# Optimization experiments

Measured on AMD Instinct MI355X. Metric: run time of the kernel, lower is better.

The kernel has to match this reference:

```python
import jax, jax.numpy as jnp
import numpy as np

B, T, H = 256, 48, 512   # batch, timesteps, hidden (= size_seq feature dim)
S = H                    # size_seq == hidden feature dim (dim_seq_in = S+1)
K = 4                    # k_wk_ahead


def setup_inputs() -> dict:
    key = jax.random.key(0)
    ks = jax.random.split(key, 20)
    g = lambda k, shp: (jax.random.normal(k, shp, dtype=jnp.float32) * 0.05)
    inp = {
        "hiddens": jax.random.normal(ks[0], (B, T, S), dtype=jnp.float32),
        "allys": jax.random.normal(ks[1], (B, T), dtype=jnp.float32),
        "k_wk_ahead": K,
        # InputAttention params (Linear stored as [in, out])
        "Wh": g(ks[2], (H, S)), "bh": g(ks[3], (S,)),
        "Ws": g(ks[4], (S, S)), "bs": g(ks[5], (S,)),
        "Wo": g(ks[6], (S, 1)), "bo": g(ks[7], (1,)),
        # GRU params (torch layout: [3H, in]/[3H, H], gates ordered r,z,n)
        "W_ih": g(ks[8], (3 * H, S + 1)), "W_hh": g(ks[9], (3 * H, H)),
        "b_ih": g(ks[10], (3 * H,)), "b_hh": g(ks[11], (3 * H,)),
        # out_layer MLP: H->H/2->H/4->H/8->1 with LeakyReLU after each
        "W1": g(ks[12], (H, H // 2)), "b1": g(ks[13], (H // 2,)),
        "W2": g(ks[14], (H // 2, H // 4)), "b2": g(ks[15], (H // 4,)),
        "W3": g(ks[16], (H // 4, H // 8)), "b3": g(ks[17], (H // 8,)),
        "W4": g(ks[18], (H // 8, 1)), "b4": g(ks[19], (1,)),
    }
    return inp


def _gru_step(x, h, W_ih, W_hh, b_ih, b_hh):
    # torch GRU cell: gates ordered (reset, update, new)
    gi = x @ W_ih.T + b_ih          # [B, 3H]
    gh = h @ W_hh.T + b_hh          # [B, 3H]
    ir, iz, inn = jnp.split(gi, 3, axis=-1)
    hr, hz, hn = jnp.split(gh, 3, axis=-1)
    r = jax.nn.sigmoid(ir + hr)
    z = jax.nn.sigmoid(iz + hz)
    n = jnp.tanh(inn + r * hn)
    return (1.0 - z) * n + z * h


def reference(hiddens, allys, k_wk_ahead, Wh, bh, Ws, bs, Wo, bo,
              W_ih, W_hh, b_ih, b_hh, W1, b1, W2, b2, W3, b3, W4, b4):
    Bb, Tt, Ss = hiddens.shape
    # linearSignals(hiddens) is time-step-invariant: precompute once
    ls = hiddens @ Ws + bs                      # [B, T, S]

    def step(d_prev, ally_t):
        lh = d_prev @ Wh + bh                   # [B, S]
        e = jnp.tanh(lh[:, None, :] + ls) @ Wo + bo    # [B, T, 1]
        att = jax.nn.softmax(e, axis=1)[..., 0]        # [B, T]
        c = jnp.einsum('bt,bts->bs', att, hiddens)     # [B, S]
        x = jnp.concatenate([c, ally_t[:, None]], axis=1)   # [B, S+1]
        d = _gru_step(x, d_prev, W_ih, W_hh, b_ih, b_hh)
        return d, c

    d0 = jnp.zeros((Bb, W_hh.shape[1]), dtype=hiddens.dtype)
    d_last, cs = jax.lax.scan(step, d0, jnp.swapaxes(allys, 0, 1))
    c_last = cs[-1]                             # c_vectors[:, -1]

    def mlp(d):
        h = jax.nn.leaky_relu(d @ W1 + b1)
        h = jax.nn.leaky_relu(h @ W2 + b2)
        h = jax.nn.leaky_relu(h @ W3 + b3)
        return jax.nn.leaky_relu(h @ W4 + b4)   # dropout is identity in eval

    outs = []
    last_d = d_last
    for _ in range(k_wk_ahead):
        out = mlp(last_d)                       # [B, 1]
        outs.append(out)
        x = jnp.concatenate([c_last, out], axis=1)
        last_d = _gru_step(x, last_d, W_ih, W_hh, b_ih, b_hh)
    return jnp.stack(outs, axis=1)[..., 0]      # [B, K]
```

## Files before the change

### kernel.cpp

```cpp
#include <hip/hip_runtime.h>
#include <cstdio>

#ifndef __has_builtin
#define __has_builtin(x) 0
#endif

#define NB      256
#define NT      48
#define NS      512
#define KAHEAD  4
#define NTHREADS 1024
#define NBLOCKS  256
#define GSIZE    32
#define RSTRIDE  544
#define XSLOT    512
#define XROWB    1088

#define WS_D     0
#define WS_X     139264
#define WS_LH    278528
#define WS_BAR   409600
#define WS_WA    409856
#define WS_WC    934144
#define WS_WN    1196288
#define WS_WS    1327360
#define WS_FLOATS 1458432

#define L_XHI    0
#define L_XLO    34816
#define L_LSB    69632
#define L_GH     118784
#define L_GI     125312
#define L_LH     131840
#define L_WO     133888
#define L_E      135936
#define L_ATT    136192
#define L_CP     136448
#define L_H1P    138496
#define L_H1S    142592
#define L_H2P    143616
#define L_H2S    145664
#define L_H3P    146176
#define L_MISC   147200
#define L_PB     147216
#define LDS_BYTES 155408

typedef float    f4v  __attribute__((ext_vector_type(4)));
typedef float    f16v __attribute__((ext_vector_type(16)));
typedef _Float16 h4v  __attribute__((ext_vector_type(4)));
typedef _Float16 h8v  __attribute__((ext_vector_type(8)));

__device__ __forceinline__ f16v MFMA32(h8v a, h8v b, f16v c) {
    return __builtin_amdgcn_mfma_f32_32x32x16_f16(a, b, c, 0, 0, 0);
}
__device__ __forceinline__ f4v MFMA16(h8v a, h8v b, f4v c) {
    return __builtin_amdgcn_mfma_f32_16x16x32_f16(a, b, c, 0, 0, 0);
}

__device__ __forceinline__ float frcp_(float x) {
#if __has_builtin(__builtin_amdgcn_rcpf)
    return __builtin_amdgcn_rcpf(x);
#else
    return 1.0f / x;
#endif
}
__device__ __forceinline__ float ftanh_(float x) {
    float e = __expf(2.0f * x);
    return 1.0f - 2.0f * frcp_(e + 1.0f);
}
__device__ __forceinline__ float fsig_(float x) { return frcp_(1.0f + __expf(-x)); }
__device__ __forceinline__ float lrelu_(float x) { return fmaxf(x, 0.01f * x); }
__device__ __forceinline__ unsigned short rne16_(unsigned u) {
    return (unsigned short)((u + 0x7FFFu + ((u >> 16) & 1u)) >> 16);
}
__device__ __forceinline__ float bf2f_(unsigned short b) {
    return __uint_as_float(((unsigned)b) << 16);
}
__device__ __forceinline__ void split16_(float v, _Float16& hi, _Float16& lo) {
    _Float16 h = (_Float16)v;
    hi = h;
    lo = (_Float16)(v - (float)h);
}

__device__ __forceinline__ void cstore1(float* p, float v) {
    asm volatile("global_store_dword %0, %1, off sc0 nt" :: "v"(p), "v"(v) : "memory");
}
__device__ __forceinline__ f4v cload4(const float* p) {
    f4v v;
    asm volatile("global_load_dwordx4 %0, %1, off sc0" : "=v"(v) : "v"(p));
    return v;
}
__device__ __forceinline__ float cload1(const float* p) {
    float v;
    asm volatile("global_load_dword %0, %1, off sc0" : "=v"(v) : "v"(p));
    return v;
}
__device__ __forceinline__ void cwait() {
    asm volatile("s_waitcnt vmcnt(0)" ::: "memory");
    __builtin_amdgcn_sched_barrier(0);
}

__device__ __forceinline__ void gbar(unsigned* bar, unsigned* epoch) {
    asm volatile("s_waitcnt vmcnt(0)" ::: "memory");
    __syncthreads();
    if (threadIdx.x == 0) {
        *epoch += GSIZE;
        __hip_atomic_fetch_add(bar, 1u, __ATOMIC_RELAXED, __HIP_MEMORY_SCOPE_AGENT);
        unsigned target = *epoch;
        int guard = 0;
        while (__hip_atomic_load(bar, __ATOMIC_RELAXED, __HIP_MEMORY_SCOPE_AGENT) < target) {
#if __has_builtin(__builtin_amdgcn_s_sleep)
            __builtin_amdgcn_s_sleep(2);
#endif
            if (++guard > (1 << 16)) break;
        }
    }
    __syncthreads();
}

__device__ __forceinline__ void cvtStore_(char* hiB, char* loB, int idx, f4v v) {
    unsigned row = (unsigned)idx / 544u;
    unsigned col = (unsigned)idx - row * 544u;
    h4v h, l;
    #pragma unroll
    for (int i = 0; i < 4; ++i) { _Float16 hh, ll; split16_(v[i], hh, ll); h[i] = hh; l[i] = ll; }
    *(h4v*)(hiB + row * XROWB + col * 2) = h;
    *(h4v*)(loB + row * XROWB + col * 2) = l;
}
__device__ __forceinline__ void stagePanel(const float* __restrict__ gsrc,
                                           char* __restrict__ hiB,
                                           char* __restrict__ loB, int tid) {
    f4v v0 = cload4(gsrc + tid * 4);
    f4v v1 = cload4(gsrc + 4096 + tid * 4);
    f4v v2 = cload4(gsrc + 8192 + tid * 4);
    f4v v3 = cload4(gsrc + 12288 + tid * 4);
    f4v v4 = {0.f, 0.f, 0.f, 0.f};
    if (tid < 256) v4 = cload4(gsrc + 16384 + tid * 4);
    cwait();
    cvtStore_(hiB, loB, tid * 4, v0);
    cvtStore_(hiB, loB, 4096 + tid * 4, v1);
    cvtStore_(hiB, loB, 8192 + tid * 4, v2);
    cvtStore_(hiB, loB, 12288 + tid * 4, v3);
    if (tid < 256) cvtStore_(hiB, loB, 16384 + tid * 4, v4);
}

__device__ __forceinline__ void gemmA(const char* smem, const _Float16* WA_,
        int cix, int g, int tid, float* ghs, float* lhw, float* pbuf,
        const float* bh, const float* bhh, bool doLH) {
    const int w = tid >> 6, l = tid & 63;
    const int nt2 = w & 1, kc = w >> 1;
    f16v acc = {0,0,0,0,0,0,0,0,0,0,0,0,0,0,0,0};
    if (w < 4) {
        const int aoff = (l & 31) * XROWB + ((l >> 5) << 4);
        const _Float16* Bp = WA_ + ((long)((cix * 2 + nt2) * 32 + kc * 16)) * 512 + (l << 3);
        #pragma unroll 4
        for (int kt = 0; kt < 16; ++kt) {
            h8v ah = *(const h8v*)(smem + L_XHI + aoff + (kc * 16 + kt) * 32);
            h8v al = *(const h8v*)(smem + L_XLO + aoff + (kc * 16 + kt) * 32);
            h8v b  = *(const h8v*)(Bp + kt * 512);
            acc = MFMA32(ah, b, acc);
            acc = MFMA32(al, b, acc);
        }
        if (kc == 1) {
            #pragma unroll
            for (int r = 0; r < 16; ++r) pbuf[nt2 * 1024 + r * 64 + l] = acc[r];
        }
    }
    __syncthreads();
    if (w < 2) {
        #pragma unroll
        for (int r = 0; r < 16; ++r) acc[r] += pbuf[nt2 * 1024 + r * 64 + l];
        const int c = nt2 * 32 + (l & 31);
        const int rb = (l >> 5) << 2;
        if (c < 16) {
            if (doLH) {
                const int j = cix * 16 + c;
                const float b = bh[j];
                #pragma unroll
                for (int r = 0; r < 16; ++r) {
                    int row = (r & 3) + ((r >> 2) << 3) + rb;
                    cstore1(lhw + (long)(g * 32 + row) * NS + j, acc[r] + b);
                }
            }
        } else {
            const int gate = (c - 16) >> 4, jj = (c - 16) & 15;
            const float b = bhh[gate * 512 + cix * 16 + jj];
            #pragma unroll
            for (int r = 0; r < 16; ++r) {
                int row = (r & 3) + ((r >> 2) << 3) + rb;
                ghs[gate * 544 + row * 17 + jj] = acc[r] + b;
            }
        }
    }
}

__device__ __forceinline__ void gemmC(const char* smem, const _Float16* WC_,
        const _Float16* WN_, int cix, int tid, float* gis, float* pbuf,
        const float* bih) {
    const int w = tid >> 6, l = tid & 63;
    f16v acc = {0,0,0,0,0,0,0,0,0,0,0,0,0,0,0,0};
    f4v an0 = {0.f,0.f,0.f,0.f}, an1 = {0.f,0.f,0.f,0.f};
    if (w < 2) {
        const int aoff = (l & 31) * XROWB + ((l >> 5) << 4);
        const _Float16* Bp = WC_ + ((long)(cix * 32 + w * 16)) * 512 + (l << 3);
        #pragma unroll 4
        for (int kt = 0; kt < 16; ++kt) {
            h8v ah = *(const h8v*)(smem + L_XHI + aoff + (w * 16 + kt) * 32);
            h8v al = *(const h8v*)(smem + L_XLO + aoff + (w * 16 + kt) * 32);
            h8v b  = *(const h8v*)(Bp + kt * 512);
            acc = MFMA32(ah, b, acc);
            acc = MFMA32(al, b, acc);
        }
        if (w == 1) {
            #pragma unroll
            for (int r = 0; r < 16; ++r) pbuf[r * 64 + l] = acc[r];
        }
    } else if (w < 4) {
        const int kc = w - 2;
        const _Float16* Bp = WN_ + ((long)(cix * 16 + kc * 8)) * 512 + (l << 3);
        const int a0 = (l & 15) * XROWB + ((l >> 4) << 4);
        const int a1 = (16 + (l & 15)) * XROWB + ((l >> 4) << 4);
        #pragma unroll 4
        for (int kt = 0; kt < 8; ++kt) {
            const int kb = (kc * 8 + kt) * 64;
            h8v b   = *(const h8v*)(Bp + kt * 512);
            h8v ah0 = *(const h8v*)(smem + L_XHI + a0 + kb);
            h8v al0 = *(const h8v*)(smem + L_XLO + a0 + kb);
            h8v ah1 = *(const h8v*)(smem + L_XHI + a1 + kb);
            h8v al1 = *(const h8v*)(smem + L_XLO + a1 + kb);
            an0 = MFMA16(ah0, b, an0); an0 = MFMA16(al0, b, an0);
            an1 = MFMA16(ah1, b, an1); an1 = MFMA16(al1, b, an1);
        }
        if (kc == 1) {
            #pragma unroll
            for (int r = 0; r < 4; ++r) {
                pbuf[1024 + r * 64 + l] = an0[r];
                pbuf[1280 + r * 64 + l] = an1[r];
            }
        }
    }
    __syncthreads();
    if (w == 0) {
        #pragma unroll
        for (int r = 0; r < 16; ++r) acc[r] += pbuf[r * 64 + l];
        const int c = l & 31, gate = c >> 4, jj = c & 15;
        const int rb = (l >> 5) << 2;
        const float b = bih[gate * 512 + cix * 16 + jj];
        #pragma unroll
        for (int r = 0; r < 16; ++r) {
            int row = (r & 3) + ((r >> 2) << 3) + rb;
            gis[gate * 544 + row * 17 + jj] = acc[r] + b;
        }
    } else if (w == 2) {
        const int jj = l & 15;
        const float b = bih[1024 + cix * 16 + jj];
        #pragma unroll
        for (int r = 0; r < 4; ++r) {
            int row = ((l >> 4) << 2) + r;
            gis[1088 + row * 17 + jj] = an0[r] + pbuf[1024 + r * 64 + l] + b;
            gis[1088 + (16 + row) * 17 + jj] = an1[r] + pbuf[1280 + r * 64 + l] + b;
        }
    }
}

__device__ __forceinline__ void lsGemm(const char* smem, const _Float16* WS_,
        int tid, int ch, unsigned short* lsb, const float* bs) {
    const int w = tid >> 6, l = tid & 63;
    const int mt = w & 1, ng = w >> 1;
    const int aoff = (mt * 16 + (l & 15)) * XROWB + ((l >> 4) << 4);
    f4v acc[4] = {{0,0,0,0},{0,0,0,0},{0,0,0,0},{0,0,0,0}};
    for (int kt = 0; kt < 16; ++kt) {
        h8v ah = *(const h8v*)(smem + L_XHI + aoff + kt * 64);
        h8v al = *(const h8v*)(smem + L_XLO + aoff + kt * 64);
        #pragma unroll
        for (int i = 0; i < 4; ++i) {
            const _Float16* bp = WS_ + ((long)((ng * 4 + i) * 16 + kt)) * 512 + (l << 3);
            h8v bb = *(const h8v*)bp;
            acc[i] = MFMA16(ah, bb, acc[i]);
            acc[i] = MFMA16(al, bb, acc[i]);
        }
    }
    #pragma unroll
    for (int i = 0; i < 4; ++i) {
        const int n = (ng * 4 + i) * 16 + (l & 15);
        const float bsv = bs[n];
        #pragma unroll
        for (int r = 0; r < 4; ++r) {
            int row = mt * 16 + ((l >> 4) << 2) + r;
            if (row < 24)
                lsb[(ch * 24 + row) * NS + n] = rne16_(__float_as_uint(acc[i][r] + bsv));
        }
    }
}

__global__ void prep_kernel(const float* __restrict__ Whh,
                            const float* __restrict__ Wih,
                            const float* __restrict__ Wh,
                            const float* __restrict__ Ws,
                            float* __restrict__ ws) {
    long i = (long)blockIdx.x * blockDim.x + threadIdx.x;
    long stride = (long)gridDim.x * blockDim.x;
    _Float16* wa = (_Float16*)(ws + WS_WA);
    _Float16* wc = (_Float16*)(ws + WS_WC);
    _Float16* wn = (_Float16*)(ws + WS_WN);
    _Float16* wsls = (_Float16*)(ws + WS_WS);

    for (long p = i; p < 131072; p += stride) {
        int l = (int)(p & 63);
        long t = p >> 6;
        int kt = (int)(t & 31);
        int u = (int)(t >> 5);
        int nt = u & 1, cix = u >> 1;
        int c = nt * 32 + (l & 31);
        #pragma unroll
        for (int e = 0; e < 8; ++e) {
            int k = kt * 16 + ((l >> 5) << 3) + e;
            float wv;
            if (c < 16) wv = Wh[(long)k * 512 + cix * 16 + c];
            else {
                int gate = (c - 16) >> 4, j = cix * 16 + ((c - 16) & 15);
                wv = Whh[((long)(gate * 512 + j)) * 512 + k];
            }
            wa[p * 8 + e] = (_Float16)wv;
        }
    }
    for (long p = i; p < 65536; p += stride) {
        int l = (int)(p & 63);
        long t = p >> 6;
        int kt = (int)(t & 31), cix = (int)(t >> 5);
        int c = l & 31, gate = c >> 4, j = cix * 16 + (c & 15);
        #pragma unroll
        for (int e = 0; e < 8; ++e) {
            int k = kt * 16 + ((l >> 5) << 3) + e;
            wc[p * 8 + e] = (_Float16)Wih[((long)(gate * 512 + j)) * 513 + k];
        }
    }
    for (long p = i; p < 32768; p += stride) {
        int l = (int)(p & 63);
        long t = p >> 6;
        int kt = (int)(t & 15), cix = (int)(t >> 4);
        int j = cix * 16 + (l & 15);
        #pragma unroll
        for (int e = 0; e < 8; ++e) {
            int k = kt * 32 + ((l >> 4) << 3) + e;
            wn[p * 8 + e] = (_Float16)Wih[((long)(1024 + j)) * 513 + k];
        }
    }
    for (long p = i; p < 32768; p += stride) {
        int l = (int)(p & 63);
        long t = p >> 6;
        int kt = (int)(t & 15), nt = (int)(t >> 4);
        int n = nt * 16 + (l & 15);
        #pragma unroll
        for (int e = 0; e < 8; ++e) {
            int k = kt * 32 + ((l >> 4) << 3) + e;
            wsls[p * 8 + e] = (_Float16)Ws[(long)k * 512 + n];
        }
    }
    for (long p = i; p < 278528; p += stride) ws[WS_D + p] = 0.0f;
    if (i < 256) ((unsigned*)(ws + WS_BAR))[i] = 0u;
}

__global__ void __launch_bounds__(NTHREADS, 4) fused_kernel(
        const float* __restrict__ hiddens, const float* __restrict__ allys,
        const float* __restrict__ bs,
        const float* __restrict__ Wo, const float* __restrict__ bo,
        const float* __restrict__ bh,
        const float* __restrict__ b_ih, const float* __restrict__ b_hh,
        const float* __restrict__ Wih,
        const float* __restrict__ W1, const float* __restrict__ b1,
        const float* __restrict__ W2, const float* __restrict__ b2,
        const float* __restrict__ W3, const float* __restrict__ b3,
        const float* __restrict__ W4, const float* __restrict__ b4,
        float* __restrict__ ws, float* __restrict__ out) {
    const int tid = threadIdx.x;

    float* dw  = ws + WS_D;
    float* xw  = ws + WS_X;
    float* lhw = ws + WS_LH;
    const _Float16* waF = (const _Float16*)(ws + WS_WA);
    const _Float16* wcF = (const _Float16*)(ws + WS_WC);
    const _Float16* wnF = (const _Float16*)(ws + WS_WN);
    const _Float16* wsF = (const _Float16*)(ws + WS_WS);
    unsigned* barbase = (unsigned*)(ws + WS_BAR);

    extern __shared__ char smem[];
    char*           xhi   = smem + L_XHI;
    char*           xlo   = smem + L_XLO;
    unsigned short* lsb   = (unsigned short*)(smem + L_LSB);
    float*          ghs   = (float*)(smem + L_GH);
    float*          gis   = (float*)(smem + L_GI);
    float*          lh_s  = (float*)(smem + L_LH);
    float*          wo_s  = (float*)(smem + L_WO);
    float*          e_s   = (float*)(smem + L_E);
    float*          att_s = (float*)(smem + L_ATT);
    float*          cp_s  = (float*)(smem + L_CP);
    float*          h1p   = (float*)(smem + L_H1P);
    float*          h1s   = (float*)(smem + L_H1S);
    float*          h2p   = (float*)(smem + L_H2P);
    float*          h2s   = (float*)(smem + L_H2S);
    float*          h3p   = (float*)(smem + L_H3P);
    int*            misc  = (int*)(smem + L_MISC);
    float*          pbuf  = (float*)(smem + L_PB);

    if (tid == 0) {
        unsigned xcc;
        asm volatile("s_getreg_b32 %0, hwreg(HW_REG_XCC_ID)" : "=s"(xcc));
        int gx = (int)(xcc & 7u);
        unsigned rk = __hip_atomic_fetch_add(barbase + gx * 32 + 1, 1u,
                                             __ATOMIC_RELAXED, __HIP_MEMORY_SCOPE_AGENT);
        misc[0] = gx;
        misc[1] = (int)(rk & 31u);
    }
    __syncthreads();
    const int g = misc[0], cix = misc[1];
    const int myb = g * 32 + cix;
    unsigned* bar = barbase + (g << 5);
    unsigned epoch = 0;

    const int sS = tid & 511, th = tid >> 9;
    const int rowE = tid >> 4, jE = tid & 15;
    const int jgE = cix * 16 + jE;
    const float* gPanelD = dw + (long)g * GSIZE * RSTRIDE;
    const float* gPanelX = xw + (long)g * GSIZE * RSTRIDE;

    float w512r = 0.f, w512z = 0.f, w512n = 0.f;
    if (tid < 512) {
        w512r = Wih[(long)jgE * 513 + 512];
        w512z = Wih[(long)(512 + jgE) * 513 + 512];
        w512n = Wih[(long)(1024 + jgE) * 513 + 512];
    }

    float hreg[24];
    if (tid < NS) wo_s[tid] = Wo[tid];
    #pragma unroll
    for (int q = 0; q < 24; ++q)
        hreg[q] = hiddens[((long)myb * NT + th * 24 + q) * NS + sS];

    for (int i = tid; i < 4352; i += NTHREADS) *(f4v*)(smem + i * 16) = (f4v){0,0,0,0};
    for (int ch = 0; ch < 2; ++ch) {
        __syncthreads();
        {
            const float* src = hiddens + ((long)myb * NT + ch * 24) * NS;
            const int i0 = tid * 12;
            #pragma unroll
            for (int j3 = 0; j3 < 3; ++j3) {
                int idx = i0 + j3 * 4;
                f4v v = *(const f4v*)(src + idx);
                int row = idx >> 9, col = idx & 511;
                h4v h, l;
                #pragma unroll
                for (int e = 0; e < 4; ++e) { _Float16 hh, ll; split16_(v[e], hh, ll); h[e] = hh; l[e] = ll; }
                *(h4v*)(xhi + row * XROWB + col * 2) = h;
                *(h4v*)(xlo + row * XROWB + col * 2) = l;
            }
        }
        __syncthreads();
        lsGemm(smem, wsF, tid, ch, lsb, bs);
    }
    __syncthreads();

    const float bo0 = bo[0];

    for (int t = 0; t < NT; ++t) {
        stagePanel(gPanelD, xhi, xlo, tid);
        __syncthreads();
        gemmA(smem, waF, cix, g, tid, ghs, lhw, pbuf, bh, b_hh, true);
        gbar(bar, &epoch);

        if (tid < 128) {
            f4v v = cload4(lhw + (long)myb * NS + tid * 4);
            cwait();
            *(f4v*)(lh_s + tid * 4) = v;
        }
        if (tid == 0) cstore1(xw + (long)myb * RSTRIDE + XSLOT, allys[myb * NT + t]);
        __syncthreads();
        {
            const int wv = tid >> 6, ln = tid & 63;
            for (int q = 0; q < 3; ++q) {
                const int tt = wv * 3 + q;
                float p = 0.f;
                #pragma unroll
                for (int i2 = 0; i2 < 8; ++i2) {
                    int s = ln + (i2 << 6);
                    p = fmaf(wo_s[s], ftanh_(lh_s[s] + bf2f_(lsb[tt * NS + s])), p);
                }
                #pragma unroll
                for (int off = 32; off >= 1; off >>= 1) p += __shfl_xor(p, off, 64);
                if (ln == 0) e_s[tt] = p + bo0;
            }
        }
        __syncthreads();
        if (tid < 64) {
            float v = (tid < NT) ? e_s[tid] : -1e30f;
            float m = v;
            #pragma unroll
            for (int off = 32; off >= 1; off >>= 1) m = fmaxf(m, __shfl_xor(m, off, 64));
            float ex = (tid < NT) ? __expf(v - m) : 0.0f;
            float ssum = ex;
            #pragma unroll
            for (int off = 32; off >= 1; off >>= 1) ssum += __shfl_xor(ssum, off, 64);
            if (tid < NT) att_s[tid] = ex * frcp_(ssum);
        }
        __syncthreads();
        {
            float p = 0.f;
            #pragma unroll
            for (int q = 0; q < 24; ++q) p = fmaf(att_s[th * 24 + q], hreg[q], p);
            if (th == 0) cp_s[sS] = p;
            __syncthreads();
            if (th == 1) cstore1(xw + (long)myb * RSTRIDE + sS, p + cp_s[sS]);
        }
        gbar(bar, &epoch);

        float hp = 0.f;
        if (tid < 512) hp = cload1(dw + (long)(g * 32 + rowE) * RSTRIDE + jgE);
        stagePanel(gPanelX, xhi, xlo, tid);
        __syncthreads();
        gemmC(smem, wcF, wnF, cix, tid, gis, pbuf, b_ih);
        __syncthreads();
        if (tid < 512) {
            float x512f = (float)*(const _Float16*)(xhi + rowE * XROWB + 1024)
                        + (float)*(const _Float16*)(xlo + rowE * XROWB + 1024);
            float gr  = gis[rowE * 17 + jE]       + ghs[rowE * 17 + jE]       + x512f * w512r;
            float gz  = gis[544 + rowE * 17 + jE] + ghs[544 + rowE * 17 + jE] + x512f * w512z;
            float gni = gis[1088 + rowE * 17 + jE] + x512f * w512n;
            float gnh = ghs[1088 + rowE * 17 + jE];
            float rg = fsig_(gr);
            float zg = fsig_(gz);
            float ng = ftanh_(gni + rg * gnh);
            cstore1(dw + (long)(g * 32 + rowE) * RSTRIDE + jgE, (1.f - zg) * ng + zg * hp);
        }
        gbar(bar, &epoch);
    }

    for (int kk = 0; kk < KAHEAD; ++kk) {
        {
            float v = 0.f;
            if (tid < NS) v = cload1(dw + (long)myb * RSTRIDE + tid);
            cwait();
            if (tid < NS) lh_s[tid] = v;
        }
        __syncthreads();
        {
            int n = tid & 255, q4 = tid >> 8;
            const float* av = lh_s + q4 * 128;
            const float* wp = W1 + (long)(q4 * 128) * 256 + n;
            float acc = 0.f;
            #pragma unroll 4
            for (int k2 = 0; k2 < 128; ++k2) { acc = fmaf(av[k2], wp[0], acc); wp += 256; }
            h1p[n * 4 + q4] = acc;
        }
        __syncthreads();
        if (tid < 256) {
            float v = h1p[tid * 4] + h1p[tid * 4 + 1] + h1p[tid * 4 + 2] + h1p[tid * 4 + 3];
            h1s[tid] = lrelu_(v + b1[tid]);
        }
        __syncthreads();
        if (tid < 512) {
            int n = tid & 127, q4 = tid >> 7;
            const float* av = h1s + q4 * 64;
            const float* wp = W2 + (long)(q4 * 64) * 128 + n;
            float acc = 0.f;
            #pragma unroll 4
            for (int k2 = 0; k2 < 64; ++k2) { acc = fmaf(av[k2], wp[0], acc); wp += 128; }
            h2p[n * 4 + q4] = acc;
        }
        __syncthreads();
        if (tid < 128) {
            float v = h2p[tid * 4] + h2p[tid * 4 + 1] + h2p[tid * 4 + 2] + h2p[tid * 4 + 3];
            h2s[tid] = lrelu_(v + b2[tid]);
        }
        __syncthreads();
        if (tid < 256) {
            int n = tid & 63, q4 = tid >> 6;
            const float* av = h2s + q4 * 32;
            const float* wp = W3 + (long)(q4 * 32) * 64 + n;
            float acc = 0.f;
            #pragma unroll 4
            for (int k2 = 0; k2 < 32; ++k2) { acc = fmaf(av[k2], wp[0], acc); wp += 64; }
            h3p[n * 4 + q4] = acc;
        }
        __syncthreads();
        if (tid < 64) {
            float v = h3p[tid * 4] + h3p[tid * 4 + 1] + h3p[tid * 4 + 2] + h3p[tid * 4 + 3];
            float h3v = lrelu_(v + b3[tid]);
            float p = h3v * W4[tid];
            #pragma unroll
            for (int off = 32; off >= 1; off >>= 1) p += __shfl_xor(p, off, 64);
            if (tid == 0) {
                float o = lrelu_(p + b4[0]);
                out[myb * KAHEAD + kk] = o;
                cstore1(xw + (long)myb * RSTRIDE + XSLOT, o);
            }
        }
        if (kk < KAHEAD - 1) {
            gbar(bar, &epoch);
            float hp = 0.f;
            if (tid < 512) hp = cload1(dw + (long)(g * 32 + rowE) * RSTRIDE + jgE);
            stagePanel(gPanelD, xhi, xlo, tid);
            __syncthreads();
            gemmA(smem, waF, cix, g, tid, ghs, lhw, pbuf, bh, b_hh, false);
            __syncthreads();
            stagePanel(gPanelX, xhi, xlo, tid);
            __syncthreads();
            gemmC(smem, wcF, wnF, cix, tid, gis, pbuf, b_ih);
            __syncthreads();
            if (tid < 512) {
                float x512f = (float)*(const _Float16*)(xhi + rowE * XROWB + 1024)
                            + (float)*(const _Float16*)(xlo + rowE * XROWB + 1024);
                float gr  = gis[rowE * 17 + jE]       + ghs[rowE * 17 + jE]       + x512f * w512r;
                float gz  = gis[544 + rowE * 17 + jE] + ghs[544 + rowE * 17 + jE] + x512f * w512z;
                float gni = gis[1088 + rowE * 17 + jE] + x512f * w512n;
                float gnh = ghs[1088 + rowE * 17 + jE];
                float rg = fsig_(gr);
                float zg = fsig_(gz);
                float ng = ftanh_(gni + rg * gnh);
                cstore1(dw + (long)(g * 32 + rowE) * RSTRIDE + jgE, (1.f - zg) * ng + zg * hp);
            }
            gbar(bar, &epoch);
        }
    }
}

extern "C" void kernel_launch(void* const* d_in, const int* in_sizes, int n_in,
                              void* d_out, int out_size, void* d_ws, size_t ws_size,
                              hipStream_t stream) {
    const float* hiddens = (const float*)d_in[0];
    const float* allys   = (const float*)d_in[1];
    const float* Wh   = (const float*)d_in[3];
    const float* bh   = (const float*)d_in[4];
    const float* Ws   = (const float*)d_in[5];
    const float* bs   = (const float*)d_in[6];
    const float* Wo   = (const float*)d_in[7];
    const float* bo   = (const float*)d_in[8];
    const float* W_ih = (const float*)d_in[9];
    const float* W_hh = (const float*)d_in[10];
    const float* b_ih = (const float*)d_in[11];
    const float* b_hh = (const float*)d_in[12];
    const float* W1 = (const float*)d_in[13];
    const float* b1 = (const float*)d_in[14];
    const float* W2 = (const float*)d_in[15];
    const float* b2 = (const float*)d_in[16];
    const float* W3 = (const float*)d_in[17];
    const float* b3 = (const float*)d_in[18];
    const float* W4 = (const float*)d_in[19];
    const float* b4 = (const float*)d_in[20];
    float* wsf = (float*)d_ws;
    float* outf = (float*)d_out;

    if (ws_size < (size_t)WS_FLOATS * sizeof(float)) {
        fprintf(stderr, "kernel_launch: workspace too small (%zu < %zu)\n",
                ws_size, (size_t)WS_FLOATS * sizeof(float));
        return;
    }

    prep_kernel<<<dim3(2048), dim3(256), 0, stream>>>(W_hh, W_ih, Wh, Ws, wsf);

    (void)hipFuncSetAttribute((const void*)fused_kernel,
                              hipFuncAttributeMaxDynamicSharedMemorySize, LDS_BYTES);

    void* args[] = { &hiddens, &allys, &bs, &Wo, &bo, &bh,
                     &b_ih, &b_hh, &W_ih, &W1, &b1, &W2, &b2, &W3, &b3, &W4, &b4,
                     &wsf, &outf };
    hipError_t e = hipLaunchCooperativeKernel((void*)fused_kernel,
                                              dim3(NBLOCKS), dim3(NTHREADS),
                                              args, LDS_BYTES, stream);
    if (e != hipSuccess) {
        fprintf(stderr, "coop launch failed (%d); plain fallback\n", (int)e);
        (void)hipGetLastError();
        fused_kernel<<<dim3(NBLOCKS), dim3(NTHREADS), LDS_BYTES, stream>>>(
            hiddens, allys, bs, Wo, bo, bh, b_ih, b_hh, W_ih,
            W1, b1, W2, b2, W3, b3, W4, b4, wsf, outf);
    }
}
```

Before: 2.018 ms.

## Keep GEMM weight fragments resident in registers and reassign warps per GEMM

```diff
diff --git a/kernel.cpp b/kernel.cpp
--- a/kernel.cpp
+++ b/kernel.cpp
@@ -57,6 +57,16 @@
     return __builtin_amdgcn_mfma_f32_16x16x32_f16(a, b, c, 0, 0, 0);
 }
 
+#if __has_builtin(__builtin_bit_cast)
+#define F2H_BITS(v) __builtin_bit_cast(h8v, (v))
+#define H2F_BITS(v) __builtin_bit_cast(f4v, (v))
+#else
+__device__ __forceinline__ h8v f2h_bits_(f4v v) { union { f4v f; h8v h; } u; u.f = v; return u.h; }
+__device__ __forceinline__ f4v h2f_bits_(h8v v) { union { f4v f; h8v h; } u; u.h = v; return u.f; }
+#define F2H_BITS(v) f2h_bits_(v)
+#define H2F_BITS(v) h2f_bits_(v)
+#endif
+
 __device__ __forceinline__ float frcp_(float x) {
 #if __has_builtin(__builtin_amdgcn_rcpf)
     return __builtin_amdgcn_rcpf(x);
@@ -144,124 +154,113 @@
     if (tid < 256) cvtStore_(hiB, loB, 16384 + tid * 4, v4);
 }
 
-__device__ __forceinline__ void gemmA(const char* smem, const _Float16* WA_,
-        int cix, int g, int tid, float* ghs, float* lhw, float* pbuf,
-        const float* bh, const float* bhh, bool doLH) {
-    const int w = tid >> 6, l = tid & 63;
-    const int nt2 = w & 1, kc = w >> 1;
-    f16v acc = {0,0,0,0,0,0,0,0,0,0,0,0,0,0,0,0};
-    if (w < 4) {
-        const int aoff = (l & 31) * XROWB + ((l >> 5) << 4);
-        const _Float16* Bp = WA_ + ((long)((cix * 2 + nt2) * 32 + kc * 16)) * 512 + (l << 3);
-        #pragma unroll 4
-        for (int kt = 0; kt < 16; ++kt) {
-            h8v ah = *(const h8v*)(smem + L_XHI + aoff + (kc * 16 + kt) * 32);
-            h8v al = *(const h8v*)(smem + L_XLO + aoff + (kc * 16 + kt) * 32);
-            h8v b  = *(const h8v*)(Bp + kt * 512);
-            acc = MFMA32(ah, b, acc);
-            acc = MFMA32(al, b, acc);
-        }
-        if (kc == 1) {
-            #pragma unroll
-            for (int r = 0; r < 16; ++r) pbuf[nt2 * 1024 + r * 64 + l] = acc[r];
-        }
-    }
-    __syncthreads();
-    if (w < 2) {
-        #pragma unroll
-        for (int r = 0; r < 16; ++r) acc[r] += pbuf[nt2 * 1024 + r * 64 + l];
-        const int c = nt2 * 32 + (l & 31);
-        const int rb = (l >> 5) << 2;
-        if (c < 16) {
-            if (doLH) {
-                const int j = cix * 16 + c;
-                const float b = bh[j];
-                #pragma unroll
-                for (int r = 0; r < 16; ++r) {
-                    int row = (r & 3) + ((r >> 2) << 3) + rb;
-                    cstore1(lhw + (long)(g * 32 + row) * NS + j, acc[r] + b);
-                }
-            }
-        } else {
-            const int gate = (c - 16) >> 4, jj = (c - 16) & 15;
-            const float b = bhh[gate * 512 + cix * 16 + jj];
-            #pragma unroll
-            for (int r = 0; r < 16; ++r) {
-                int row = (r & 3) + ((r >> 2) << 3) + rb;
-                ghs[gate * 544 + row * 17 + jj] = acc[r] + b;
-            }
-        }
-    }
-}
-
-__device__ __forceinline__ void gemmC(const char* smem, const _Float16* WC_,
-        const _Float16* WN_, int cix, int tid, float* gis, float* pbuf,
-        const float* bih) {
-    const int w = tid >> 6, l = tid & 63;
-    f16v acc = {0,0,0,0,0,0,0,0,0,0,0,0,0,0,0,0};
-    f4v an0 = {0.f,0.f,0.f,0.f}, an1 = {0.f,0.f,0.f,0.f};
-    if (w < 2) {
-        const int aoff = (l & 31) * XROWB + ((l >> 5) << 4);
-        const _Float16* Bp = WC_ + ((long)(cix * 32 + w * 16)) * 512 + (l << 3);
-        #pragma unroll 4
-        for (int kt = 0; kt < 16; ++kt) {
-            h8v ah = *(const h8v*)(smem + L_XHI + aoff + (w * 16 + kt) * 32);
-            h8v al = *(const h8v*)(smem + L_XLO + aoff + (w * 16 + kt) * 32);
-            h8v b  = *(const h8v*)(Bp + kt * 512);
-            acc = MFMA32(ah, b, acc);
-            acc = MFMA32(al, b, acc);
-        }
-        if (w == 1) {
-            #pragma unroll
-            for (int r = 0; r < 16; ++r) pbuf[r * 64 + l] = acc[r];
-        }
-    } else if (w < 4) {
-        const int kc = w - 2;
-        const _Float16* Bp = WN_ + ((long)(cix * 16 + kc * 8)) * 512 + (l << 3);
-        const int a0 = (l & 15) * XROWB + ((l >> 4) << 4);
-        const int a1 = (16 + (l & 15)) * XROWB + ((l >> 4) << 4);
-        #pragma unroll 4
-        for (int kt = 0; kt < 8; ++kt) {
-            const int kb = (kc * 8 + kt) * 64;
-            h8v b   = *(const h8v*)(Bp + kt * 512);
-            h8v ah0 = *(const h8v*)(smem + L_XHI + a0 + kb);
-            h8v al0 = *(const h8v*)(smem + L_XLO + a0 + kb);
-            h8v ah1 = *(const h8v*)(smem + L_XHI + a1 + kb);
-            h8v al1 = *(const h8v*)(smem + L_XLO + a1 + kb);
-            an0 = MFMA16(ah0, b, an0); an0 = MFMA16(al0, b, an0);
-            an1 = MFMA16(ah1, b, an1); an1 = MFMA16(al1, b, an1);
-        }
-        if (kc == 1) {
-            #pragma unroll
-            for (int r = 0; r < 4; ++r) {
-                pbuf[1024 + r * 64 + l] = an0[r];
-                pbuf[1280 + r * 64 + l] = an1[r];
-            }
-        }
-    }
-    __syncthreads();
-    if (w == 0) {
-        #pragma unroll
-        for (int r = 0; r < 16; ++r) acc[r] += pbuf[r * 64 + l];
-        const int c = l & 31, gate = c >> 4, jj = c & 15;
-        const int rb = (l >> 5) << 2;
-        const float b = bih[gate * 512 + cix * 16 + jj];
-        #pragma unroll
-        for (int r = 0; r < 16; ++r) {
-            int row = (r & 3) + ((r >> 2) << 3) + rb;
-            gis[gate * 544 + row * 17 + jj] = acc[r] + b;
-        }
-    } else if (w == 2) {
-        const int jj = l & 15;
-        const float b = bih[1024 + cix * 16 + jj];
-        #pragma unroll
-        for (int r = 0; r < 4; ++r) {
-            int row = ((l >> 4) << 2) + r;
-            gis[1088 + row * 17 + jj] = an0[r] + pbuf[1024 + r * 64 + l] + b;
-            gis[1088 + (16 + row) * 17 + jj] = an1[r] + pbuf[1280 + r * 64 + l] + b;
-        }
-    }
-}
+#define DO_GEMMA(doLH) do {                                                          \
+    f16v acc_ = (f16v){0,0,0,0,0,0,0,0,0,0,0,0,0,0,0,0};                             \
+    if (w < 4) {                                                                     \
+        const int kc_ = w >> 1;                                                      \
+        const int aoff_ = (l & 31) * XROWB + ((l >> 5) << 4);                        \
+        _Pragma("unroll")                                                            \
+        for (int kt = 0; kt < 16; ++kt) {                                            \
+            h8v ah = *(const h8v*)(smem + L_XHI + aoff_ + (kc_ * 16 + kt) * 32);     \
+            h8v al = *(const h8v*)(smem + L_XLO + aoff_ + (kc_ * 16 + kt) * 32);     \
+            acc_ = MFMA32(ah, wreg[kt], acc_);                                       \
+            acc_ = MFMA32(al, wreg[kt], acc_);                                       \
+        }                                                                            \
+        if (kc_ == 1) {                                                              \
+            _Pragma("unroll")                                                        \
+            for (int r = 0; r < 16; ++r) pbuf[(w & 1) * 1024 + r * 64 + l] = acc_[r];\
+        }                                                                            \
+    }                                                                                \
+    __syncthreads();                                                                 \
+    if (w < 2) {                                                                     \
+        _Pragma("unroll")                                                            \
+        for (int r = 0; r < 16; ++r) acc_[r] += pbuf[w * 1024 + r * 64 + l];         \
+        const int c_ = w * 32 + (l & 31);                                            \
+        const int rb_ = (l >> 5) << 2;                                               \
+        if (c_ < 16) {                                                               \
+            if (doLH) {                                                              \
+                const int j_ = cix * 16 + c_;                                        \
+                const float bb_ = bh[j_];                                            \
+                _Pragma("unroll")                                                    \
+                for (int r = 0; r < 16; ++r) {                                       \
+                    int row_ = (r & 3) + ((r >> 2) << 3) + rb_;                      \
+                    cstore1(lhw + (long)(g * 32 + row_) * NS + j_, acc_[r] + bb_);   \
+                }                                                                    \
+            }                                                                        \
+        } else {                                                                     \
+            const int gate_ = (c_ - 16) >> 4, jj_ = (c_ - 16) & 15;                  \
+            const float bb_ = b_hh[gate_ * 512 + cix * 16 + jj_];                    \
+            _Pragma("unroll")                                                        \
+            for (int r = 0; r < 16; ++r) {                                           \
+                int row_ = (r & 3) + ((r >> 2) << 3) + rb_;                          \
+                ghs[gate_ * 544 + row_ * 17 + jj_] = acc_[r] + bb_;                  \
+            }                                                                        \
+        }                                                                            \
+    }                                                                                \
+} while (0)
+
+#define DO_GEMMC() do {                                                              \
+    f16v acc_ = (f16v){0,0,0,0,0,0,0,0,0,0,0,0,0,0,0,0};                             \
+    f4v an0_ = {0.f,0.f,0.f,0.f}, an1_ = {0.f,0.f,0.f,0.f};                          \
+    if (w == 4 || w == 5) {                                                          \
+        const int kc_ = w - 4;                                                       \
+        const int aoff_ = (l & 31) * XROWB + ((l >> 5) << 4);                        \
+        _Pragma("unroll")                                                            \
+        for (int kt = 0; kt < 16; ++kt) {                                            \
+            h8v ah = *(const h8v*)(smem + L_XHI + aoff_ + (kc_ * 16 + kt) * 32);     \
+            h8v al = *(const h8v*)(smem + L_XLO + aoff_ + (kc_ * 16 + kt) * 32);     \
+            acc_ = MFMA32(ah, wreg[kt], acc_);                                       \
+            acc_ = MFMA32(al, wreg[kt], acc_);                                       \
+        }                                                                            \
+        if (kc_ == 1) {                                                              \
+            _Pragma("unroll")                                                        \
+            for (int r = 0; r < 16; ++r) pbuf[r * 64 + l] = acc_[r];                 \
+        }                                                                            \
+    } else if (w == 6 || w == 7) {                                                   \
+        const int kc_ = w - 6;                                                       \
+        const int a0_ = (l & 15) * XROWB + ((l >> 4) << 4);                          \
+        const int a1_ = a0_ + 16 * XROWB;                                            \
+        _Pragma("unroll")                                                            \
+        for (int kt = 0; kt < 8; ++kt) {                                             \
+            const int kb_ = (kc_ * 8 + kt) * 64;                                     \
+            h8v ah0 = *(const h8v*)(smem + L_XHI + a0_ + kb_);                       \
+            h8v al0 = *(const h8v*)(smem + L_XLO + a0_ + kb_);                       \
+            h8v ah1 = *(const h8v*)(smem + L_XHI + a1_ + kb_);                       \
+            h8v al1 = *(const h8v*)(smem + L_XLO + a1_ + kb_);                       \
+            an0_ = MFMA16(ah0, wreg[kt], an0_); an0_ = MFMA16(al0, wreg[kt], an0_);  \
+            an1_ = MFMA16(ah1, wreg[kt], an1_); an1_ = MFMA16(al1, wreg[kt], an1_);  \
+        }                                                                            \
+        if (kc_ == 1) {                                                              \
+            _Pragma("unroll")                                                        \
+            for (int r = 0; r < 4; ++r) {                                            \
+                pbuf[1024 + r * 64 + l] = an0_[r];                                   \
+                pbuf[1280 + r * 64 + l] = an1_[r];                                   \
+            }                                                                        \
+        }                                                                            \
+    }                                                                                \
+    __syncthreads();                                                                 \
+    if (w == 4) {                                                                    \
+        _Pragma("unroll")                                                            \
+        for (int r = 0; r < 16; ++r) acc_[r] += pbuf[r * 64 + l];                    \
+        const int c_ = l & 31, gate_ = c_ >> 4, jj_ = c_ & 15;                       \
+        const int rb_ = (l >> 5) << 2;                                               \
+        const float bb_ = b_ih[gate_ * 512 + cix * 16 + jj_];                        \
+        _Pragma("unroll")                                                            \
+        for (int r = 0; r < 16; ++r) {                                               \
+            int row_ = (r & 3) + ((r >> 2) << 3) + rb_;                              \
+            gis[gate_ * 544 + row_ * 17 + jj_] = acc_[r] + bb_;                      \
+        }                                                                            \
+    } else if (w == 6) {                                                             \
+        const int jj_ = l & 15;                                                      \
+        const float bb_ = b_ih[1024 + cix * 16 + jj_];                               \
+        _Pragma("unroll")                                                            \
+        for (int r = 0; r < 4; ++r) {                                                \
+            int row_ = ((l >> 4) << 2) + r;                                          \
+            gis[1088 + row_ * 17 + jj_] = an0_[r] + pbuf[1024 + r * 64 + l] + bb_;   \
+            gis[1088 + (16 + row_) * 17 + jj_] = an1_[r] + pbuf[1280 + r * 64 + l] + bb_; \
+        }                                                                            \
+    }                                                                                \
+} while (0)
 
 __device__ __forceinline__ void lsGemm(const char* smem, const _Float16* WS_,
         int tid, int ch, unsigned short* lsb, const float* bs) {
@@ -394,7 +393,6 @@
     float*          wo_s  = (float*)(smem + L_WO);
     float*          e_s   = (float*)(smem + L_E);
     float*          att_s = (float*)(smem + L_ATT);
-    float*          cp_s  = (float*)(smem + L_CP);
     float*          h1p   = (float*)(smem + L_H1P);
     float*          h1s   = (float*)(smem + L_H1S);
     float*          h2p   = (float*)(smem + L_H2P);
@@ -418,6 +416,7 @@
     unsigned* bar = barbase + (g << 5);
     unsigned epoch = 0;
 
+    const int w = tid >> 6, l = tid & 63;
     const int sS = tid & 511, th = tid >> 9;
     const int rowE = tid >> 4, jE = tid & 15;
     const int jgE = cix * 16 + jE;
@@ -431,11 +430,7 @@
         w512n = Wih[(long)(1024 + jgE) * 513 + 512];
     }
 
-    float hreg[24];
     if (tid < NS) wo_s[tid] = Wo[tid];
-    #pragma unroll
-    for (int q = 0; q < 24; ++q)
-        hreg[q] = hiddens[((long)myb * NT + th * 24 + q) * NS + sS];
 
     for (int i = tid; i < 4352; i += NTHREADS) *(f4v*)(smem + i * 16) = (f4v){0,0,0,0};
     for (int ch = 0; ch < 2; ++ch) {
@@ -448,24 +443,47 @@
                 int idx = i0 + j3 * 4;
                 f4v v = *(const f4v*)(src + idx);
                 int row = idx >> 9, col = idx & 511;
-                h4v h, l;
+                h4v h, lo;
                 #pragma unroll
-                for (int e = 0; e < 4; ++e) { _Float16 hh, ll; split16_(v[e], hh, ll); h[e] = hh; l[e] = ll; }
+                for (int e = 0; e < 4; ++e) { _Float16 hh, ll; split16_(v[e], hh, ll); h[e] = hh; lo[e] = ll; }
                 *(h4v*)(xhi + row * XROWB + col * 2) = h;
-                *(h4v*)(xlo + row * XROWB + col * 2) = l;
+                *(h4v*)(xlo + row * XROWB + col * 2) = lo;
             }
         }
         __syncthreads();
         lsGemm(smem, wsF, tid, ch, lsb, bs);
     }
     __syncthreads();
+
+    h8v wreg[16];
+    if (w < 4) {
+        const _Float16* p = waF + ((long)((cix * 2 + (w & 1)) * 32 + (w >> 1) * 16)) * 512 + (l << 3);
+        #pragma unroll
+        for (int kt = 0; kt < 16; ++kt) wreg[kt] = *(const h8v*)(p + kt * 512);
+    } else if (w < 6) {
+        const _Float16* p = wcF + ((long)(cix * 32 + (w - 4) * 16)) * 512 + (l << 3);
+        #pragma unroll
+        for (int kt = 0; kt < 16; ++kt) wreg[kt] = *(const h8v*)(p + kt * 512);
+    } else if (w < 8) {
+        const _Float16* p = wnF + ((long)(cix * 16 + (w - 6) * 8)) * 512 + (l << 3);
+        #pragma unroll
+        for (int kt = 0; kt < 8; ++kt) wreg[kt] = *(const h8v*)(p + kt * 512);
+    } else {
+        const float* hb = hiddens + (long)myb * NT * NS + sS;
+        #pragma unroll
+        for (int q = 0; q < 12; ++q) {
+            f4v v = { hb[(q * 4 + 0) * 512], hb[(q * 4 + 1) * 512],
+                      hb[(q * 4 + 2) * 512], hb[(q * 4 + 3) * 512] };
+            wreg[q] = F2H_BITS(v);
+        }
+    }
 
     const float bo0 = bo[0];
 
     for (int t = 0; t < NT; ++t) {
         stagePanel(gPanelD, xhi, xlo, tid);
         __syncthreads();
-        gemmA(smem, waF, cix, g, tid, ghs, lhw, pbuf, bh, b_hh, true);
+        DO_GEMMA(true);
         gbar(bar, &epoch);
 
         if (tid < 128) {
@@ -503,13 +521,17 @@
             if (tid < NT) att_s[tid] = ex * frcp_(ssum);
         }
         __syncthreads();
-        {
-            float p = 0.f;
+        if (tid >= 512) {
+            float c = 0.f;
             #pragma unroll
-            for (int q = 0; q < 24; ++q) p = fmaf(att_s[th * 24 + q], hreg[q], p);
-            if (th == 0) cp_s[sS] = p;
-            __syncthreads();
-            if (th == 1) cstore1(xw + (long)myb * RSTRIDE + sS, p + cp_s[sS]);
+            for (int q = 0; q < 12; ++q) {
+                f4v hv = H2F_BITS(wreg[q]);
+                c = fmaf(att_s[q * 4 + 0], hv.x, c);
+                c = fmaf(att_s[q * 4 + 1], hv.y, c);
+                c = fmaf(att_s[q * 4 + 2], hv.z, c);
+                c = fmaf(att_s[q * 4 + 3], hv.w, c);
+            }
+            cstore1(xw + (long)myb * RSTRIDE + sS, c);
         }
         gbar(bar, &epoch);
 
@@ -517,7 +539,7 @@
         if (tid < 512) hp = cload1(dw + (long)(g * 32 + rowE) * RSTRIDE + jgE);
         stagePanel(gPanelX, xhi, xlo, tid);
         __syncthreads();
-        gemmC(smem, wcF, wnF, cix, tid, gis, pbuf, b_ih);
+        DO_GEMMC();
         __syncthreads();
         if (tid < 512) {
             float x512f = (float)*(const _Float16*)(xhi + rowE * XROWB + 1024)
@@ -600,11 +622,11 @@
             if (tid < 512) hp = cload1(dw + (long)(g * 32 + rowE) * RSTRIDE + jgE);
             stagePanel(gPanelD, xhi, xlo, tid);
             __syncthreads();
-            gemmA(smem, waF, cix, g, tid, ghs, lhw, pbuf, bh, b_hh, false);
+            DO_GEMMA(false);
             __syncthreads();
             stagePanel(gPanelX, xhi, xlo, tid);
             __syncthreads();
-            gemmC(smem, wcF, wnF, cix, tid, gis, pbuf, b_ih);
+            DO_GEMMC();
             __syncthreads();
             if (tid < 512) {
                 float x512f = (float)*(const _Float16*)(xhi + rowE * XROWB + 1024)
```

Result: faster. 1.812 ms (-10.2%).
